# Kernel optimization log

Measured on AMD Instinct MI355X. Metric: run time of the kernel, lower is better.

The kernel has to match this reference:

```python
import jax, jax.numpy as jnp
import numpy as np

NEG_SLOPE = 0.2


def gat_layer(x, src, dst, W, a_src, a_dst, b, heads, out_c, concat):
    N = x.shape[0]
    h = (x @ W).reshape(N, heads, out_c)                      # [N,H,C]
    alpha_s = jnp.einsum('nhc,hc->nh', h, a_src)              # [N,H]
    alpha_d = jnp.einsum('nhc,hc->nh', h, a_dst)              # [N,H]
    e = jax.nn.leaky_relu(alpha_s[src] + alpha_d[dst], NEG_SLOPE)  # [E,H]
    # softmax over incoming edges per destination node (segment softmax)
    m = jax.ops.segment_max(e, dst, num_segments=N)
    m = jnp.where(jnp.isfinite(m), m, 0.0)
    ex = jnp.exp(e - m[dst])
    denom = jax.ops.segment_sum(ex, dst, num_segments=N)
    alpha = ex / (denom[dst] + 1e-16)                         # [E,H]
    out = jax.ops.segment_sum(alpha[:, :, None] * h[src], dst, num_segments=N)  # [N,H,C]
    out = out.reshape(N, heads * out_c) if concat else out.mean(axis=1)
    return out + b


def setup_inputs() -> dict:
    key = jax.random.key(0)
    ks = jax.random.split(key, 12)
    N, E, D, H, C, G = 20000, 160000, 256, 4, 128, 64
    x = jax.random.normal(ks[0], (N, D), dtype=jnp.float32)
    edge_index = jax.random.randint(ks[1], (2, E), 0, N)
    batch = jnp.sort(jax.random.randint(ks[2], (N,), 0, G))
    s = 0.05
    params = {
        'W1': jax.random.normal(ks[3], (D, H * C), jnp.float32) * s,
        'a_src1': jax.random.normal(ks[4], (H, C), jnp.float32) * s,
        'a_dst1': jax.random.normal(ks[5], (H, C), jnp.float32) * s,
        'b1': jnp.zeros((H * C,), jnp.float32),
        'W2': jax.random.normal(ks[6], (H * C, C), jnp.float32) * s,
        'a_src2': jax.random.normal(ks[7], (1, C), jnp.float32) * s,
        'a_dst2': jax.random.normal(ks[8], (1, C), jnp.float32) * s,
        'b2': jnp.zeros((C,), jnp.float32),
        'fc1_W': jax.random.normal(ks[9], (C, C // 2), jnp.float32) * s,
        'fc1_b': jnp.zeros((C // 2,), jnp.float32),
        'fc2_W': jax.random.normal(ks[10], (C // 2, 1), jnp.float32) * s,
        'fc2_b': jnp.zeros((1,), jnp.float32),
    }
    return dict(x=x, edge_index=edge_index, batch=batch, **params)


def reference(x, edge_index, batch, W1, a_src1, a_dst1, b1, W2, a_src2, a_dst2, b2,
              fc1_W, fc1_b, fc2_W, fc2_b):
    N = x.shape[0]
    G = 64  # number of graphs
    # add self-loops (PyG GATConv default)
    loop = jnp.arange(N, dtype=edge_index.dtype)
    src = jnp.concatenate([edge_index[0], loop])
    dst = jnp.concatenate([edge_index[1], loop])
    h = jax.nn.relu(gat_layer(x, src, dst, W1, a_src1, a_dst1, b1, 4, 128, True))
    h = gat_layer(h, src, dst, W2, a_src2, a_dst2, b2, 1, 128, False)
    # global mean pool per graph
    sums = jax.ops.segment_sum(h, batch, num_segments=G)
    cnts = jax.ops.segment_sum(jnp.ones((N,), h.dtype), batch, num_segments=G)
    pooled = sums / jnp.maximum(cnts, 1.0)[:, None]          # [G,128]
    out = jax.nn.relu(pooled @ fc1_W + fc1_b)
    return out @ fc2_W + fc2_b                                # [G,1]
```

## Files before the change

kernel.cpp:

```cpp
#include <hip/hip_runtime.h>
#include <hip/hip_bf16.h>
#include <cstdint>
#include <cstddef>

#define NEG_SLOPE 0.2f

typedef __attribute__((ext_vector_type(8))) __bf16 bf16x8;
typedef __attribute__((ext_vector_type(4))) __bf16 bf16x4;
typedef __attribute__((ext_vector_type(2))) __bf16 bf16x2;
typedef __attribute__((ext_vector_type(4))) float  f32x4;

__device__ __forceinline__ float lrelu(float v) {
    return (v < 0.f) ? NEG_SLOPE * v : v;
}

__device__ __forceinline__ unsigned fkey(float x) {
    unsigned b = __float_as_uint(x);
    return b ^ (unsigned)(((int)b >> 31) | 0x80000000);
}
__device__ __forceinline__ float funkey(unsigned k) {
    unsigned b = (k & 0x80000000u) ? (k ^ 0x80000000u) : ~k;
    return __uint_as_float(b);
}

__global__ __launch_bounds__(256) void gemm2_sum(
    const __bf16* __restrict__ A,
    const __bf16* __restrict__ Bt,
    __bf16* __restrict__ Cout,
    const float* __restrict__ ps_part, const float* __restrict__ pd_part,
    float* __restrict__ as2, float* __restrict__ ad2,
    unsigned* __restrict__ gmax2u,
    int M, int MB)
{
    if ((int)blockIdx.y >= MB) {
        int chunk = ((int)blockIdx.y - MB) * 2 + (int)blockIdx.x;
        int i = chunk * 256 + threadIdx.x;
        float lm = -1e30f;
        if (i < M) {
            float4 p = *(const float4*)&ps_part[(size_t)i * 4];
            float4 q = *(const float4*)&pd_part[(size_t)i * 4];
            float s = (p.x + p.y) + (p.z + p.w);
            float d = (q.x + q.y) + (q.z + q.w);
            as2[i] = s;
            ad2[i] = d;
            lm = s;
        }
        #pragma unroll
        for (int t = 1; t < 64; t <<= 1) lm = fmaxf(lm, __shfl_xor(lm, t));
        if ((threadIdx.x & 63) == 0) atomicMax(gmax2u, fkey(lm));
        return;
    }

    const int tid  = threadIdx.x;
    const int wave = tid >> 6, lane = tid & 63;
    const int wr = wave >> 1, wc = wave & 1;
    const int rowbase = blockIdx.y * 64 + wr * 32;
    const int colbase = blockIdx.x * 64 + wc * 32;
    const int l15 = lane & 15, kg = lane >> 4;
    const int K = 512, N = 128;

    size_t aoff[2], boff[2];
    #pragma unroll
    for (int mf = 0; mf < 2; ++mf) {
        int r = rowbase + mf * 16 + l15;
        if (r > M - 1) r = M - 1;
        aoff[mf] = (size_t)r * K + kg * 8;
    }
    #pragma unroll
    for (int nf = 0; nf < 2; ++nf) {
        int c = colbase + nf * 16 + l15;
        boff[nf] = (size_t)c * K + kg * 8;
    }

    f32x4 acc[2][2];
    #pragma unroll
    for (int mf = 0; mf < 2; ++mf)
        #pragma unroll
        for (int nf = 0; nf < 2; ++nf)
            acc[mf][nf] = (f32x4){0.f, 0.f, 0.f, 0.f};

    #pragma unroll 2
    for (int k0 = 0; k0 < K; k0 += 32) {
        bf16x8 af[2], bfr[2];
        #pragma unroll
        for (int mf = 0; mf < 2; ++mf)
            af[mf] = *(const bf16x8*)(A + aoff[mf] + k0);
        #pragma unroll
        for (int nf = 0; nf < 2; ++nf)
            bfr[nf] = *(const bf16x8*)(Bt + boff[nf] + k0);
        #pragma unroll
        for (int mf = 0; mf < 2; ++mf)
            #pragma unroll
            for (int nf = 0; nf < 2; ++nf)
                acc[mf][nf] = __builtin_amdgcn_mfma_f32_16x16x32_bf16(af[mf], bfr[nf], acc[mf][nf], 0, 0, 0);
    }

    #pragma unroll
    for (int mf = 0; mf < 2; ++mf)
        #pragma unroll
        for (int j = 0; j < 4; ++j) {
            int r = rowbase + mf * 16 + kg * 4 + j;
            if (r < M) {
                #pragma unroll
                for (int nf = 0; nf < 2; ++nf) {
                    int c = colbase + nf * 16 + l15;
                    Cout[(size_t)r * N + c] = (__bf16)acc[mf][nf][j];
                }
            }
        }
}

__global__ __launch_bounds__(256) void gemm1_agg(
    const __bf16* __restrict__ aggx,
    const __bf16* __restrict__ w1t,
    const float* __restrict__ b1, const float* __restrict__ wsd2,
    __bf16* __restrict__ out1b,
    float* __restrict__ ps_part, float* __restrict__ pd_part,
    int M)
{
    const int head = blockIdx.x;
    const int tid  = threadIdx.x;
    const int wave = tid >> 6, lane = tid & 63;
    const int wr = wave >> 1, wc = wave & 1;
    const int rowbase = blockIdx.y * 64 + wr * 32;
    const int l15 = lane & 15, kg = lane >> 4;

    size_t aoff[2], boff[4];
    #pragma unroll
    for (int mf = 0; mf < 2; ++mf) {
        int r = rowbase + mf * 16 + l15;
        if (r > M - 1) r = M - 1;
        aoff[mf] = (size_t)r * 1024 + head * 256 + kg * 8;
    }
    #pragma unroll
    for (int nf = 0; nf < 4; ++nf) {
        int c = head * 128 + wc * 64 + nf * 16 + l15;
        boff[nf] = (size_t)c * 256 + kg * 8;
    }

    f32x4 acc[2][4];
    #pragma unroll
    for (int mf = 0; mf < 2; ++mf)
        #pragma unroll
        for (int nf = 0; nf < 4; ++nf)
            acc[mf][nf] = (f32x4){0.f, 0.f, 0.f, 0.f};

    #pragma unroll 2
    for (int k0 = 0; k0 < 256; k0 += 32) {
        bf16x8 af[2], bfr[4];
        #pragma unroll
        for (int mf = 0; mf < 2; ++mf)
            af[mf] = *(const bf16x8*)(aggx + aoff[mf] + k0);
        #pragma unroll
        for (int nf = 0; nf < 4; ++nf)
            bfr[nf] = *(const bf16x8*)(w1t + boff[nf] + k0);
        #pragma unroll
        for (int mf = 0; mf < 2; ++mf)
            #pragma unroll
            for (int nf = 0; nf < 4; ++nf)
                acc[mf][nf] = __builtin_amdgcn_mfma_f32_16x16x32_bf16(af[mf], bfr[nf], acc[mf][nf], 0, 0, 0);
    }

    __shared__ float smp[2][64], smd[2][64];

    #pragma unroll
    for (int mf = 0; mf < 2; ++mf)
        #pragma unroll
        for (int j = 0; j < 4; ++j) {
            int r = rowbase + mf * 16 + kg * 4 + j;
            float ps = 0.f, pd = 0.f;
            #pragma unroll
            for (int nf = 0; nf < 4; ++nf) {
                int col = head * 128 + wc * 64 + nf * 16 + l15;
                float o = fmaxf(acc[mf][nf][j] + b1[col], 0.f);
                if (r < M)
                    out1b[(size_t)r * 512 + col] = (__bf16)o;
                ps = fmaf(o, wsd2[col], ps);
                pd = fmaf(o, wsd2[512 + col], pd);
            }
            #pragma unroll
            for (int t = 1; t < 16; t <<= 1) {
                ps += __shfl_xor(ps, t);
                pd += __shfl_xor(pd, t);
            }
            if (l15 == 0) {
                int lr = wr * 32 + mf * 16 + kg * 4 + j;
                smp[wc][lr] = ps;
                smd[wc][lr] = pd;
            }
        }
    __syncthreads();
    if (tid < 64) {
        int r = blockIdx.y * 64 + tid;
        if (r < M) {
            ps_part[(size_t)r * 4 + head] = smp[0][tid] + smp[1][tid];
            pd_part[(size_t)r * 4 + head] = smd[0][tid] + smd[1][tid];
        }
    }
}

__global__ void prep_kernel(const float* __restrict__ W1, const float* __restrict__ W2,
                            const float* __restrict__ as1w, const float* __restrict__ ad1w,
                            const float* __restrict__ as2w, const float* __restrict__ ad2w,
                            const int* __restrict__ batch,
                            __bf16* __restrict__ w1t, __bf16* __restrict__ w2t,
                            float* __restrict__ wsd1, float* __restrict__ wsd2,
                            int* __restrict__ gstart, int* __restrict__ cnt,
                            unsigned* __restrict__ gmax2u,
                            int N, int G)
{
    int t = blockIdx.x * 256 + threadIdx.x;
    if (t < 131072) {
        int i = t;
        int k = i >> 9, n = i & 511;
        w1t[n * 256 + k] = (__bf16)W1[i];
    } else if (t < 196608) {
        int j = t - 131072;
        int k = j >> 7, n = j & 127;
        w2t[n * 512 + k] = (__bf16)W2[j];
    } else if (t < 199680) {
        int t2 = t - 196608;
        if (t2 < 2048) {
            int k = t2 >> 3, v = t2 & 7, h = v >> 1;
            const float* av = (v & 1) ? (ad1w + h * 128) : (as1w + h * 128);
            float s = 0.f;
            for (int c = 0; c < 128; ++c) s += W1[k * 512 + h * 128 + c] * av[c];
            wsd1[v * 256 + k] = s;
        } else {
            int t3 = t2 - 2048;
            int k = t3 >> 1, v = t3 & 1;
            const float* av = v ? ad2w : as2w;
            float s = 0.f;
            for (int c = 0; c < 128; ++c) s += W2[k * 128 + c] * av[c];
            wsd2[v * 512 + k] = s;
        }
    } else if (t < 199680 + N) {
        int n = t - 199680;
        int b    = batch[n];
        int prev = (n == 0) ? -1 : batch[n - 1];
        for (int g = prev + 1; g <= b; ++g) gstart[g] = n;
        if (n == N - 1) {
            for (int g = b + 1; g <= G; ++g) gstart[g] = N;
        }
    } else if (t < 199680 + 2 * N) {
        cnt[t - 199680 - N] = 0;
    } else if (t == 199680 + 2 * N) {
        *gmax2u = fkey(-1e30f);
    }
}

__global__ __launch_bounds__(256) void count_cvtx(
    const int* __restrict__ ei, int* __restrict__ cnt,
    const float* __restrict__ x, const float* __restrict__ wsd1,
    __bf16* __restrict__ xb, float* __restrict__ as1_, float* __restrict__ ad1_,
    int ET, int E0, int N, int CB)
{
    if ((int)blockIdx.x < CB) {
        int base = (blockIdx.x * 256 + threadIdx.x) * 2;
        #pragma unroll
        for (int k = 0; k < 2; ++k) {
            int e = base + k;
            if (e < ET) {
                int d = (e < E0) ? ei[E0 + e] : (e - E0);
                atomicAdd(&cnt[d], 1);
            }
        }
        return;
    }
    int bid = blockIdx.x - CB;
    int wave = threadIdx.x >> 6, lane = threadIdx.x & 63;
    int n = bid * 4 + wave;
    if (n >= N) return;
    float4 xv = *(const float4*)&x[(size_t)n * 256 + lane * 4];
    bf16x4 xo;
    xo[0] = (__bf16)xv.x; xo[1] = (__bf16)xv.y; xo[2] = (__bf16)xv.z; xo[3] = (__bf16)xv.w;
    *(bf16x4*)&xb[(size_t)n * 256 + lane * 4] = xo;
    float p[8];
    #pragma unroll
    for (int v = 0; v < 8; ++v) {
        float4 wv = *(const float4*)&wsd1[v * 256 + lane * 4];
        p[v] = xv.x * wv.x + xv.y * wv.y + xv.z * wv.z + xv.w * wv.w;
    }
    #pragma unroll
    for (int v = 0; v < 8; ++v)
        #pragma unroll
        for (int s = 1; s < 64; s <<= 1) p[v] += __shfl_xor(p[v], s);
    if (lane == 0) {
        #pragma unroll
        for (int h = 0; h < 4; ++h) {
            as1_[n * 4 + h] = p[2 * h];
            ad1_[n * 4 + h] = p[2 * h + 1];
        }
    }
}

__global__ __launch_bounds__(1024) void scan_gmax(
    const int* __restrict__ cnt, int* __restrict__ offs, int* __restrict__ cur,
    const float* __restrict__ as1_, float* __restrict__ gmax1, int n)
{
    constexpr int CHUNK = 20;
    int t = threadIdx.x;
    int base = t * CHUNK;
    int v[CHUNK];
    int s = 0;
    #pragma unroll
    for (int i = 0; i < CHUNK; ++i) {
        int idx = base + i;
        int xv = (idx < n) ? cnt[idx] : 0;
        v[i] = s; s += xv;
    }
    int lane = t & 63, w = t >> 6;
    int sc = s;
    #pragma unroll
    for (int d = 1; d < 64; d <<= 1) {
        int o = __shfl_up(sc, d);
        if (lane >= d) sc += o;
    }
    __shared__ int wt[16], wb[17];
    __shared__ float gsm[16][4];
    if (lane == 63) wt[w] = sc;
    __syncthreads();
    if (t == 0) {
        int acc = 0;
        for (int i = 0; i < 16; ++i) { wb[i] = acc; acc += wt[i]; }
        wb[16] = acc;
    }
    __syncthreads();
    int ebase = wb[w] + (sc - s);
    #pragma unroll
    for (int i = 0; i < CHUNK; ++i) {
        int idx = base + i;
        if (idx < n) {
            int o = ebase + v[i];
            offs[idx] = o;
            cur[idx]  = o;
        }
    }
    if (t == 0) offs[n] = wb[16];

    float lm0 = -1e30f, lm1 = -1e30f, lm2 = -1e30f, lm3 = -1e30f;
    for (int i = t; i < n; i += 1024) {
        float4 a = *(const float4*)&as1_[(size_t)i * 4];
        lm0 = fmaxf(lm0, a.x); lm1 = fmaxf(lm1, a.y);
        lm2 = fmaxf(lm2, a.z); lm3 = fmaxf(lm3, a.w);
    }
    #pragma unroll
    for (int d = 1; d < 64; d <<= 1) {
        lm0 = fmaxf(lm0, __shfl_xor(lm0, d));
        lm1 = fmaxf(lm1, __shfl_xor(lm1, d));
        lm2 = fmaxf(lm2, __shfl_xor(lm2, d));
        lm3 = fmaxf(lm3, __shfl_xor(lm3, d));
    }
    if (lane == 0) {
        gsm[w][0] = lm0; gsm[w][1] = lm1; gsm[w][2] = lm2; gsm[w][3] = lm3;
    }
    __syncthreads();
    if (t == 0) {
        float m0 = -1e30f, m1 = -1e30f, m2 = -1e30f, m3 = -1e30f;
        for (int i = 0; i < 16; ++i) {
            m0 = fmaxf(m0, gsm[i][0]); m1 = fmaxf(m1, gsm[i][1]);
            m2 = fmaxf(m2, gsm[i][2]); m3 = fmaxf(m3, gsm[i][3]);
        }
        gmax1[0] = m0; gmax1[1] = m1; gmax1[2] = m2; gmax1[3] = m3;
    }
}

__global__ void scatter_kernel(const int* __restrict__ ei, int* __restrict__ cur,
                               int* __restrict__ srcs, int ET, int E0)
{
    int e = blockIdx.x * blockDim.x + threadIdx.x;
    if (e >= ET) return;
    int d = (e < E0) ? ei[E0 + e] : (e - E0);
    int s = (e < E0) ? ei[e] : (e - E0);
    int pos = atomicAdd(&cur[d], 1);
    srcs[pos] = s;
}

__global__ __launch_bounds__(256) void aggx_kernel(
    const __bf16* __restrict__ xb, const int* __restrict__ offs,
    const int* __restrict__ srcs,
    const float* __restrict__ as1_, const float* __restrict__ ad1_,
    const float* __restrict__ gmax1,
    __bf16* __restrict__ aggx, int N)
{
    __shared__ float w4s[4][64][4];
    __shared__ int   sidx[4][64];
    int wave = threadIdx.x >> 6, lane = threadIdx.x & 63;
    int n = blockIdx.x * 4 + wave;
    if (n >= N) return;
    int s0 = offs[n], s1 = offs[n + 1];
    float4 adv = *(const float4*)&ad1_[(size_t)n * 4];
    float m0 = lrelu(gmax1[0] + adv.x);
    float m1 = lrelu(gmax1[1] + adv.y);
    float m2 = lrelu(gmax1[2] + adv.z);
    float m3 = lrelu(gmax1[3] + adv.w);

    float d0 = 0.f, d1 = 0.f, d2 = 0.f, d3 = 0.f;
    float a0[4] = {0.f,0.f,0.f,0.f}, a1[4] = {0.f,0.f,0.f,0.f};
    float a2[4] = {0.f,0.f,0.f,0.f}, a3[4] = {0.f,0.f,0.f,0.f};
    const __bf16* xbase = xb + lane * 4;

    for (int base = s0; base < s1; base += 64) {
        int cnt = min(64, s1 - base);
        if (lane < cnt) {
            int s = srcs[base + lane];
            float4 av = *(const float4*)&as1_[(size_t)s * 4];
            float w0 = __expf(lrelu(av.x + adv.x) - m0);
            float w1 = __expf(lrelu(av.y + adv.y) - m1);
            float w2 = __expf(lrelu(av.z + adv.z) - m2);
            float w3 = __expf(lrelu(av.w + adv.w) - m3);
            d0 += w0; d1 += w1; d2 += w2; d3 += w3;
            sidx[wave][lane] = s;
            w4s[wave][lane][0] = w0; w4s[wave][lane][1] = w1;
            w4s[wave][lane][2] = w2; w4s[wave][lane][3] = w3;
        }
        int j = 0;
        for (; j + 7 < cnt; j += 8) {
            int s_[8]; float4 w_[8]; bf16x4 xv_[8];
            #pragma unroll
            for (int i = 0; i < 8; ++i) {
                s_[i] = sidx[wave][j + i];
                w_[i] = *(const float4*)&w4s[wave][j + i][0];
            }
            #pragma unroll
            for (int i = 0; i < 8; ++i)
                xv_[i] = *(const bf16x4*)(xbase + (size_t)s_[i] * 256);
            #pragma unroll
            for (int i = 0; i < 8; ++i) {
                float xf[4];
                #pragma unroll
                for (int c = 0; c < 4; ++c) xf[c] = (float)xv_[i][c];
                #pragma unroll
                for (int c = 0; c < 4; ++c) {
                    a0[c] = fmaf(w_[i].x, xf[c], a0[c]);
                    a1[c] = fmaf(w_[i].y, xf[c], a1[c]);
                    a2[c] = fmaf(w_[i].z, xf[c], a2[c]);
                    a3[c] = fmaf(w_[i].w, xf[c], a3[c]);
                }
            }
        }
        for (; j < cnt; ++j) {
            int s = sidx[wave][j];
            float4 w = *(const float4*)&w4s[wave][j][0];
            bf16x4 xv = *(const bf16x4*)(xbase + (size_t)s * 256);
            float xf[4];
            #pragma unroll
            for (int c = 0; c < 4; ++c) xf[c] = (float)xv[c];
            #pragma unroll
            for (int c = 0; c < 4; ++c) {
                a0[c] = fmaf(w.x, xf[c], a0[c]);
                a1[c] = fmaf(w.y, xf[c], a1[c]);
                a2[c] = fmaf(w.z, xf[c], a2[c]);
                a3[c] = fmaf(w.w, xf[c], a3[c]);
            }
        }
    }

    #pragma unroll
    for (int t = 1; t < 64; t <<= 1) {
        d0 += __shfl_xor(d0, t);
        d1 += __shfl_xor(d1, t);
        d2 += __shfl_xor(d2, t);
        d3 += __shfl_xor(d3, t);
    }

    float i0 = 1.f / (d0 + 1e-16f);
    float i1 = 1.f / (d1 + 1e-16f);
    float i2 = 1.f / (d2 + 1e-16f);
    float i3 = 1.f / (d3 + 1e-16f);
    __bf16* obase = aggx + (size_t)n * 1024 + lane * 4;
    bf16x4 o;
    #pragma unroll
    for (int c = 0; c < 4; ++c) o[c] = (__bf16)(a0[c] * i0);
    *(bf16x4*)(obase + 0)   = o;
    #pragma unroll
    for (int c = 0; c < 4; ++c) o[c] = (__bf16)(a1[c] * i1);
    *(bf16x4*)(obase + 256) = o;
    #pragma unroll
    for (int c = 0; c < 4; ++c) o[c] = (__bf16)(a2[c] * i2);
    *(bf16x4*)(obase + 512) = o;
    #pragma unroll
    for (int c = 0; c < 4; ++c) o[c] = (__bf16)(a3[c] * i3);
    *(bf16x4*)(obase + 768) = o;
}

__global__ __launch_bounds__(256) void aggregate2_kernel(
    const __bf16* __restrict__ h2b, const int* __restrict__ offs,
    const int* __restrict__ srcs,
    const float* __restrict__ as2, const float* __restrict__ ad2,
    const unsigned* __restrict__ gmax2u,
    const float* __restrict__ b2, float* __restrict__ out2, int N)
{
    __shared__ float wls[4][64];
    __shared__ int   sidx[4][64];
    int wave = threadIdx.x >> 6, lane = threadIdx.x & 63;
    int n = blockIdx.x * 4 + wave;
    if (n >= N) return;
    int s0 = offs[n], s1 = offs[n + 1];
    float adn = ad2[n];
    float m = lrelu(funkey(*gmax2u) + adn);

    float den = 0.f;
    float c0 = 0.f, c1 = 0.f;
    const __bf16* hbase = h2b + lane * 2;

    for (int base = s0; base < s1; base += 64) {
        int cnt = min(64, s1 - base);
        if (lane < cnt) {
            int s = srcs[base + lane];
            float w = __expf(lrelu(as2[s] + adn) - m);
            den += w;
            sidx[wave][lane] = s;
            wls[wave][lane]  = w;
        }
        int j = 0;
        for (; j + 7 < cnt; j += 8) {
            int s_[8]; float w_[8]; bf16x2 h_[8];
            #pragma unroll
            for (int i = 0; i < 8; ++i) {
                s_[i] = sidx[wave][j + i];
                w_[i] = wls[wave][j + i];
            }
            #pragma unroll
            for (int i = 0; i < 8; ++i)
                h_[i] = *(const bf16x2*)(hbase + (size_t)s_[i] * 128);
            #pragma unroll
            for (int i = 0; i < 8; ++i) {
                c0 = fmaf(w_[i], (float)h_[i][0], c0);
                c1 = fmaf(w_[i], (float)h_[i][1], c1);
            }
        }
        for (; j < cnt; ++j) {
            int s = sidx[wave][j];
            float w = wls[wave][j];
            bf16x2 hv = *(const bf16x2*)(hbase + (size_t)s * 128);
            c0 = fmaf(w, (float)hv[0], c0);
            c1 = fmaf(w, (float)hv[1], c1);
        }
    }

    #pragma unroll
    for (int t = 1; t < 64; t <<= 1) den += __shfl_xor(den, t);
    float inv = 1.f / (den + 1e-16f);
    float2 o;
    o.x = c0 * inv + b2[lane * 2 + 0];
    o.y = c1 * inv + b2[lane * 2 + 1];
    *(float2*)&out2[(size_t)n * 128 + lane * 2] = o;
}

#define POOL_S 16
__global__ void pool_stage1(const float* __restrict__ out2, const int* __restrict__ gstart,
                            float* __restrict__ partial, int C)
{
    int g = blockIdx.x, slice = blockIdx.y;
    int c = threadIdx.x;
    int s = gstart[g], e = gstart[g + 1];
    int len = e - s;
    int chunk = (len + POOL_S - 1) / POOL_S;
    int n0 = s + slice * chunk;
    int n1 = min(n0 + chunk, e);
    float acc = 0.f;
    for (int n = n0; n < n1; ++n) acc += out2[(size_t)n * C + c];
    partial[((size_t)g * POOL_S + slice) * C + c] = acc;
}

__global__ __launch_bounds__(128) void pool_head(
    const float* __restrict__ partial, const int* __restrict__ gstart,
    const float* __restrict__ fc1W, const float* __restrict__ fc1b,
    const float* __restrict__ fc2W, const float* __restrict__ fc2b,
    float* __restrict__ out)
{
    int g = blockIdx.x;
    int t = threadIdx.x;
    __shared__ float pl[128];
    float acc = 0.f;
    #pragma unroll
    for (int s = 0; s < POOL_S; ++s)
        acc += partial[((size_t)g * POOL_S + s) * 128 + t];
    float cntf = (float)(gstart[g + 1] - gstart[g]);
    pl[t] = acc / fmaxf(cntf, 1.0f);
    __syncthreads();
    if (t < 64) {
        float v = 0.f;
        for (int c = 0; c < 128; ++c)
            v += pl[c] * fc1W[c * 64 + t];
        v = fmaxf(v + fc1b[t], 0.f) * fc2W[t];
        #pragma unroll
        for (int s = 32; s > 0; s >>= 1) v += __shfl_down(v, s);
        if (t == 0) out[g] = v + fc2b[0];
    }
}

extern "C" void kernel_launch(void* const* d_in, const int* in_sizes, int n_in,
                              void* d_out, int out_size, void* d_ws, size_t ws_size,
                              hipStream_t stream)
{
    const float* x    = (const float*)d_in[0];
    const int*   ei   = (const int*)d_in[1];
    const int*   batch= (const int*)d_in[2];
    const float* W1   = (const float*)d_in[3];
    const float* as1w = (const float*)d_in[4];
    const float* ad1w = (const float*)d_in[5];
    const float* b1   = (const float*)d_in[6];
    const float* W2   = (const float*)d_in[7];
    const float* as2w = (const float*)d_in[8];
    const float* ad2w = (const float*)d_in[9];
    const float* b2   = (const float*)d_in[10];
    const float* fc1W = (const float*)d_in[11];
    const float* fc1b = (const float*)d_in[12];
    const float* fc2W = (const float*)d_in[13];
    const float* fc2b = (const float*)d_in[14];
    float* out = (float*)d_out;

    const int D = 256, C = 128, G = 64;
    const int N  = in_sizes[0] / D;
    const int E0 = in_sizes[1] / 2;
    const int ET = E0 + N;

    char* p = (char*)d_ws;
    auto alloc = [&](size_t bytes) -> char* {
        char* r = p;
        p += (bytes + 255) & ~(size_t)255;
        return r;
    };
    __bf16* xb    = (__bf16*)alloc((size_t)N * D * 2);
    __bf16* aggx  = (__bf16*)alloc((size_t)N * 4 * 256 * 2);
    __bf16* out1b = (__bf16*)alloc((size_t)N * 512 * 2);
    __bf16* h2b   = (__bf16*)alloc((size_t)N * C * 2);
    float*  out2  = (float*)alloc((size_t)N * C * 4);
    __bf16* w1t   = (__bf16*)alloc((size_t)256 * 512 * 2);
    __bf16* w2t   = (__bf16*)alloc((size_t)512 * 128 * 2);
    float* wsd1   = (float*)alloc(8 * 256 * 4);
    float* wsd2   = (float*)alloc(2 * 512 * 4);
    float* gmax1  = (float*)alloc(4 * 4);
    unsigned* gmax2u = (unsigned*)alloc(4);
    float* as1_   = (float*)alloc((size_t)N * 4 * 4);
    float* ad1_   = (float*)alloc((size_t)N * 4 * 4);
    float* ps_part= (float*)alloc((size_t)N * 4 * 4);
    float* pd_part= (float*)alloc((size_t)N * 4 * 4);
    float* as2    = (float*)alloc((size_t)N * 4);
    float* ad2    = (float*)alloc((size_t)N * 4);
    int*   cnt    = (int*)alloc((size_t)N * 4);
    int*   cur    = (int*)alloc((size_t)N * 4);
    int*   offs   = (int*)alloc((size_t)(N + 1) * 4);
    int*   srcs   = (int*)alloc((size_t)ET * 4);
    int*   gstart = (int*)alloc((size_t)(G + 1) * 4);
    float* partial= (float*)alloc((size_t)G * POOL_S * C * 4);

    {
        int total = 199680 + 2 * N + 1;
        prep_kernel<<<(total + 255) / 256, 256, 0, stream>>>(
            W1, W2, as1w, ad1w, as2w, ad2w, batch,
            w1t, w2t, wsd1, wsd2, gstart, cnt, gmax2u, N, G);
    }

    {
        int CB = (ET + 511) / 512;
        count_cvtx<<<CB + N / 4, 256, 0, stream>>>(
            ei, cnt, x, wsd1, xb, as1_, ad1_, ET, E0, N, CB);
    }

    scan_gmax<<<1, 1024, 0, stream>>>(cnt, offs, cur, as1_, gmax1, N);

    scatter_kernel<<<(ET + 255) / 256, 256, 0, stream>>>(ei, cur, srcs, ET, E0);

    aggx_kernel<<<(N + 3) / 4, 256, 0, stream>>>(
        xb, offs, srcs, as1_, ad1_, gmax1, aggx, N);

    gemm1_agg<<<dim3(4, (N + 63) / 64), 256, 0, stream>>>(
        aggx, w1t, b1, wsd2, out1b, ps_part, pd_part, N);

    {
        int MB = (N + 63) / 64;
        int SB = ((N + 255) / 256 + 1) / 2;
        gemm2_sum<<<dim3(2, MB + SB), 256, 0, stream>>>(
            out1b, w2t, h2b, ps_part, pd_part, as2, ad2, gmax2u, N, MB);
    }

    aggregate2_kernel<<<(N + 3) / 4, 256, 0, stream>>>(
        h2b, offs, srcs, as2, ad2, gmax2u, b2, out2, N);

    pool_stage1<<<dim3(G, POOL_S), C, 0, stream>>>(out2, gstart, partial, C);
    pool_head<<<G, 128, 0, stream>>>(partial, gstart, fc1W, fc1b, fc2W, fc2b, out);
}
```

Before: 194.0 us.

## Fuse layer-1 neighbor aggregation with per-head GEMM through shared memory

Merges the aggregation kernel and the first GEMM into one kernel. Each block aggregates 16 destination nodes for all four heads into an LDS tile, then each wave runs the MFMA GEMM for one head. This removes the N×1024 bf16 aggx round trip through global memory and one kernel launch. In exchange the GEMM tile is only 16 rows, so each block reloads W1 slices with less reuse, and the sequential per-wave aggregation of four nodes may leave waves unbalanced before the barrier.

```diff
diff --git a/kernel.cpp b/kernel.cpp
--- a/kernel.cpp
+++ b/kernel.cpp
@@ -21,6 +21,173 @@
 __device__ __forceinline__ float funkey(unsigned k) {
     unsigned b = (k & 0x80000000u) ? (k ^ 0x80000000u) : ~k;
     return __uint_as_float(b);
+}
+
+__global__ __launch_bounds__(256) void agg_gemm1(
+    const __bf16* __restrict__ xb, const int* __restrict__ offs,
+    const int* __restrict__ srcs,
+    const float* __restrict__ as1_, const float* __restrict__ ad1_,
+    const float* __restrict__ gmax1,
+    const __bf16* __restrict__ w1t,
+    const float* __restrict__ b1, const float* __restrict__ wsd2,
+    __bf16* __restrict__ out1b,
+    float* __restrict__ ps_part, float* __restrict__ pd_part,
+    int N)
+{
+    __shared__ __bf16 axs[4][16][260];
+    __shared__ float w4s[4][64][4];
+    __shared__ int   sidx[4][64];
+
+    const int tid  = threadIdx.x;
+    const int wave = tid >> 6, lane = tid & 63;
+    const int tile = blockIdx.x * 16;
+
+    for (int i = 0; i < 4; ++i) {
+        int nn = wave * 4 + i;
+        int n  = tile + nn;
+        if (n >= N) break;
+        int s0 = offs[n], s1 = offs[n + 1];
+        float4 adv = *(const float4*)&ad1_[(size_t)n * 4];
+        float m0 = lrelu(gmax1[0] + adv.x);
+        float m1 = lrelu(gmax1[1] + adv.y);
+        float m2 = lrelu(gmax1[2] + adv.z);
+        float m3 = lrelu(gmax1[3] + adv.w);
+
+        float d0 = 0.f, d1 = 0.f, d2 = 0.f, d3 = 0.f;
+        float a0[4] = {0.f,0.f,0.f,0.f}, a1[4] = {0.f,0.f,0.f,0.f};
+        float a2[4] = {0.f,0.f,0.f,0.f}, a3[4] = {0.f,0.f,0.f,0.f};
+        const __bf16* xbase = xb + lane * 4;
+
+        for (int base = s0; base < s1; base += 64) {
+            int cnt = min(64, s1 - base);
+            if (lane < cnt) {
+                int s = srcs[base + lane];
+                float4 av = *(const float4*)&as1_[(size_t)s * 4];
+                float w0 = __expf(lrelu(av.x + adv.x) - m0);
+                float w1 = __expf(lrelu(av.y + adv.y) - m1);
+                float w2 = __expf(lrelu(av.z + adv.z) - m2);
+                float w3 = __expf(lrelu(av.w + adv.w) - m3);
+                d0 += w0; d1 += w1; d2 += w2; d3 += w3;
+                sidx[wave][lane] = s;
+                w4s[wave][lane][0] = w0; w4s[wave][lane][1] = w1;
+                w4s[wave][lane][2] = w2; w4s[wave][lane][3] = w3;
+            }
+            int j = 0;
+            for (; j + 7 < cnt; j += 8) {
+                int s_[8]; float4 w_[8]; bf16x4 xv_[8];
+                #pragma unroll
+                for (int q = 0; q < 8; ++q) {
+                    s_[q] = sidx[wave][j + q];
+                    w_[q] = *(const float4*)&w4s[wave][j + q][0];
+                }
+                #pragma unroll
+                for (int q = 0; q < 8; ++q)
+                    xv_[q] = *(const bf16x4*)(xbase + (size_t)s_[q] * 256);
+                #pragma unroll
+                for (int q = 0; q < 8; ++q) {
+                    float xf[4];
+                    #pragma unroll
+                    for (int c = 0; c < 4; ++c) xf[c] = (float)xv_[q][c];
+                    #pragma unroll
+                    for (int c = 0; c < 4; ++c) {
+                        a0[c] = fmaf(w_[q].x, xf[c], a0[c]);
+                        a1[c] = fmaf(w_[q].y, xf[c], a1[c]);
+                        a2[c] = fmaf(w_[q].z, xf[c], a2[c]);
+                        a3[c] = fmaf(w_[q].w, xf[c], a3[c]);
+                    }
+                }
+            }
+            for (; j < cnt; ++j) {
+                int s = sidx[wave][j];
+                float4 w = *(const float4*)&w4s[wave][j][0];
+                bf16x4 xv = *(const bf16x4*)(xbase + (size_t)s * 256);
+                float xf[4];
+                #pragma unroll
+                for (int c = 0; c < 4; ++c) xf[c] = (float)xv[c];
+                #pragma unroll
+                for (int c = 0; c < 4; ++c) {
+                    a0[c] = fmaf(w.x, xf[c], a0[c]);
+                    a1[c] = fmaf(w.y, xf[c], a1[c]);
+                    a2[c] = fmaf(w.z, xf[c], a2[c]);
+                    a3[c] = fmaf(w.w, xf[c], a3[c]);
+                }
+            }
+        }
+
+        #pragma unroll
+        for (int t = 1; t < 64; t <<= 1) {
+            d0 += __shfl_xor(d0, t);
+            d1 += __shfl_xor(d1, t);
+            d2 += __shfl_xor(d2, t);
+            d3 += __shfl_xor(d3, t);
+        }
+        float i0 = 1.f / (d0 + 1e-16f);
+        float i1 = 1.f / (d1 + 1e-16f);
+        float i2 = 1.f / (d2 + 1e-16f);
+        float i3 = 1.f / (d3 + 1e-16f);
+        bf16x4 o;
+        #pragma unroll
+        for (int c = 0; c < 4; ++c) o[c] = (__bf16)(a0[c] * i0);
+        *(bf16x4*)&axs[0][nn][lane * 4] = o;
+        #pragma unroll
+        for (int c = 0; c < 4; ++c) o[c] = (__bf16)(a1[c] * i1);
+        *(bf16x4*)&axs[1][nn][lane * 4] = o;
+        #pragma unroll
+        for (int c = 0; c < 4; ++c) o[c] = (__bf16)(a2[c] * i2);
+        *(bf16x4*)&axs[2][nn][lane * 4] = o;
+        #pragma unroll
+        for (int c = 0; c < 4; ++c) o[c] = (__bf16)(a3[c] * i3);
+        *(bf16x4*)&axs[3][nn][lane * 4] = o;
+    }
+    __syncthreads();
+
+    const int head = wave;
+    const int l15 = lane & 15, kg = lane >> 4;
+
+    f32x4 acc[8];
+    #pragma unroll
+    for (int nf = 0; nf < 8; ++nf) acc[nf] = (f32x4){0.f, 0.f, 0.f, 0.f};
+
+    #pragma unroll 2
+    for (int k0 = 0; k0 < 256; k0 += 32) {
+        bf16x4 alo = *(const bf16x4*)&axs[head][l15][k0 + kg * 8];
+        bf16x4 ahi = *(const bf16x4*)&axs[head][l15][k0 + kg * 8 + 4];
+        bf16x8 af;
+        #pragma unroll
+        for (int c = 0; c < 4; ++c) { af[c] = alo[c]; af[4 + c] = ahi[c]; }
+        bf16x8 bfr[8];
+        #pragma unroll
+        for (int nf = 0; nf < 8; ++nf)
+            bfr[nf] = *(const bf16x8*)(w1t + (size_t)(head * 128 + nf * 16 + l15) * 256 + k0 + kg * 8);
+        #pragma unroll
+        for (int nf = 0; nf < 8; ++nf)
+            acc[nf] = __builtin_amdgcn_mfma_f32_16x16x32_bf16(af, bfr[nf], acc[nf], 0, 0, 0);
+    }
+
+    #pragma unroll
+    for (int j = 0; j < 4; ++j) {
+        int nn = kg * 4 + j;
+        int r  = tile + nn;
+        float ps = 0.f, pd = 0.f;
+        #pragma unroll
+        for (int nf = 0; nf < 8; ++nf) {
+            int col = head * 128 + nf * 16 + l15;
+            float o = fmaxf(acc[nf][j] + b1[col], 0.f);
+            if (r < N)
+                out1b[(size_t)r * 512 + col] = (__bf16)o;
+            ps = fmaf(o, wsd2[col], ps);
+            pd = fmaf(o, wsd2[512 + col], pd);
+        }
+        #pragma unroll
+        for (int t = 1; t < 16; t <<= 1) {
+            ps += __shfl_xor(ps, t);
+            pd += __shfl_xor(pd, t);
+        }
+        if (l15 == 0 && r < N) {
+            ps_part[(size_t)r * 4 + head] = ps;
+            pd_part[(size_t)r * 4 + head] = pd;
+        }
+    }
 }
 
 __global__ __launch_bounds__(256) void gemm2_sum(
@@ -108,95 +275,6 @@
                 }
             }
         }
-}
-
-__global__ __launch_bounds__(256) void gemm1_agg(
-    const __bf16* __restrict__ aggx,
-    const __bf16* __restrict__ w1t,
-    const float* __restrict__ b1, const float* __restrict__ wsd2,
-    __bf16* __restrict__ out1b,
-    float* __restrict__ ps_part, float* __restrict__ pd_part,
-    int M)
-{
-    const int head = blockIdx.x;
-    const int tid  = threadIdx.x;
-    const int wave = tid >> 6, lane = tid & 63;
-    const int wr = wave >> 1, wc = wave & 1;
-    const int rowbase = blockIdx.y * 64 + wr * 32;
-    const int l15 = lane & 15, kg = lane >> 4;
-
-    size_t aoff[2], boff[4];
-    #pragma unroll
-    for (int mf = 0; mf < 2; ++mf) {
-        int r = rowbase + mf * 16 + l15;
-        if (r > M - 1) r = M - 1;
-        aoff[mf] = (size_t)r * 1024 + head * 256 + kg * 8;
-    }
-    #pragma unroll
-    for (int nf = 0; nf < 4; ++nf) {
-        int c = head * 128 + wc * 64 + nf * 16 + l15;
-        boff[nf] = (size_t)c * 256 + kg * 8;
-    }
-
-    f32x4 acc[2][4];
-    #pragma unroll
-    for (int mf = 0; mf < 2; ++mf)
-        #pragma unroll
-        for (int nf = 0; nf < 4; ++nf)
-            acc[mf][nf] = (f32x4){0.f, 0.f, 0.f, 0.f};
-
-    #pragma unroll 2
-    for (int k0 = 0; k0 < 256; k0 += 32) {
-        bf16x8 af[2], bfr[4];
-        #pragma unroll
-        for (int mf = 0; mf < 2; ++mf)
-            af[mf] = *(const bf16x8*)(aggx + aoff[mf] + k0);
-        #pragma unroll
-        for (int nf = 0; nf < 4; ++nf)
-            bfr[nf] = *(const bf16x8*)(w1t + boff[nf] + k0);
-        #pragma unroll
-        for (int mf = 0; mf < 2; ++mf)
-            #pragma unroll
-            for (int nf = 0; nf < 4; ++nf)
-                acc[mf][nf] = __builtin_amdgcn_mfma_f32_16x16x32_bf16(af[mf], bfr[nf], acc[mf][nf], 0, 0, 0);
-    }
-
-    __shared__ float smp[2][64], smd[2][64];
-
-    #pragma unroll
-    for (int mf = 0; mf < 2; ++mf)
-        #pragma unroll
-        for (int j = 0; j < 4; ++j) {
-            int r = rowbase + mf * 16 + kg * 4 + j;
-            float ps = 0.f, pd = 0.f;
-            #pragma unroll
-            for (int nf = 0; nf < 4; ++nf) {
-                int col = head * 128 + wc * 64 + nf * 16 + l15;
-                float o = fmaxf(acc[mf][nf][j] + b1[col], 0.f);
-                if (r < M)
-                    out1b[(size_t)r * 512 + col] = (__bf16)o;
-                ps = fmaf(o, wsd2[col], ps);
-                pd = fmaf(o, wsd2[512 + col], pd);
-            }
-            #pragma unroll
-            for (int t = 1; t < 16; t <<= 1) {
-                ps += __shfl_xor(ps, t);
-                pd += __shfl_xor(pd, t);
-            }
-            if (l15 == 0) {
-                int lr = wr * 32 + mf * 16 + kg * 4 + j;
-                smp[wc][lr] = ps;
-                smd[wc][lr] = pd;
-            }
-        }
-    __syncthreads();
-    if (tid < 64) {
-        int r = blockIdx.y * 64 + tid;
-        if (r < M) {
-            ps_part[(size_t)r * 4 + head] = smp[0][tid] + smp[1][tid];
-            pd_part[(size_t)r * 4 + head] = smd[0][tid] + smd[1][tid];
-        }
-    }
 }
 
 __global__ void prep_kernel(const float* __restrict__ W1, const float* __restrict__ W2,
@@ -376,114 +454,6 @@
     srcs[pos] = s;
 }
 
-__global__ __launch_bounds__(256) void aggx_kernel(
-    const __bf16* __restrict__ xb, const int* __restrict__ offs,
-    const int* __restrict__ srcs,
-    const float* __restrict__ as1_, const float* __restrict__ ad1_,
-    const float* __restrict__ gmax1,
-    __bf16* __restrict__ aggx, int N)
-{
-    __shared__ float w4s[4][64][4];
-    __shared__ int   sidx[4][64];
-    int wave = threadIdx.x >> 6, lane = threadIdx.x & 63;
-    int n = blockIdx.x * 4 + wave;
-    if (n >= N) return;
-    int s0 = offs[n], s1 = offs[n + 1];
-    float4 adv = *(const float4*)&ad1_[(size_t)n * 4];
-    float m0 = lrelu(gmax1[0] + adv.x);
-    float m1 = lrelu(gmax1[1] + adv.y);
-    float m2 = lrelu(gmax1[2] + adv.z);
-    float m3 = lrelu(gmax1[3] + adv.w);
-
-    float d0 = 0.f, d1 = 0.f, d2 = 0.f, d3 = 0.f;
-    float a0[4] = {0.f,0.f,0.f,0.f}, a1[4] = {0.f,0.f,0.f,0.f};
-    float a2[4] = {0.f,0.f,0.f,0.f}, a3[4] = {0.f,0.f,0.f,0.f};
-    const __bf16* xbase = xb + lane * 4;
-
-    for (int base = s0; base < s1; base += 64) {
-        int cnt = min(64, s1 - base);
-        if (lane < cnt) {
-            int s = srcs[base + lane];
-            float4 av = *(const float4*)&as1_[(size_t)s * 4];
-            float w0 = __expf(lrelu(av.x + adv.x) - m0);
-            float w1 = __expf(lrelu(av.y + adv.y) - m1);
-            float w2 = __expf(lrelu(av.z + adv.z) - m2);
-            float w3 = __expf(lrelu(av.w + adv.w) - m3);
-            d0 += w0; d1 += w1; d2 += w2; d3 += w3;
-            sidx[wave][lane] = s;
-            w4s[wave][lane][0] = w0; w4s[wave][lane][1] = w1;
-            w4s[wave][lane][2] = w2; w4s[wave][lane][3] = w3;
-        }
-        int j = 0;
-        for (; j + 7 < cnt; j += 8) {
-            int s_[8]; float4 w_[8]; bf16x4 xv_[8];
-            #pragma unroll
-            for (int i = 0; i < 8; ++i) {
-                s_[i] = sidx[wave][j + i];
-                w_[i] = *(const float4*)&w4s[wave][j + i][0];
-            }
-            #pragma unroll
-            for (int i = 0; i < 8; ++i)
-                xv_[i] = *(const bf16x4*)(xbase + (size_t)s_[i] * 256);
-            #pragma unroll
-            for (int i = 0; i < 8; ++i) {
-                float xf[4];
-                #pragma unroll
-                for (int c = 0; c < 4; ++c) xf[c] = (float)xv_[i][c];
-                #pragma unroll
-                for (int c = 0; c < 4; ++c) {
-                    a0[c] = fmaf(w_[i].x, xf[c], a0[c]);
-                    a1[c] = fmaf(w_[i].y, xf[c], a1[c]);
-                    a2[c] = fmaf(w_[i].z, xf[c], a2[c]);
-                    a3[c] = fmaf(w_[i].w, xf[c], a3[c]);
-                }
-            }
-        }
-        for (; j < cnt; ++j) {
-            int s = sidx[wave][j];
-            float4 w = *(const float4*)&w4s[wave][j][0];
-            bf16x4 xv = *(const bf16x4*)(xbase + (size_t)s * 256);
-            float xf[4];
-            #pragma unroll
-            for (int c = 0; c < 4; ++c) xf[c] = (float)xv[c];
-            #pragma unroll
-            for (int c = 0; c < 4; ++c) {
-                a0[c] = fmaf(w.x, xf[c], a0[c]);
-                a1[c] = fmaf(w.y, xf[c], a1[c]);
-                a2[c] = fmaf(w.z, xf[c], a2[c]);
-                a3[c] = fmaf(w.w, xf[c], a3[c]);
-            }
-        }
-    }
-
-    #pragma unroll
-    for (int t = 1; t < 64; t <<= 1) {
-        d0 += __shfl_xor(d0, t);
-        d1 += __shfl_xor(d1, t);
-        d2 += __shfl_xor(d2, t);
-        d3 += __shfl_xor(d3, t);
-    }
-
-    float i0 = 1.f / (d0 + 1e-16f);
-    float i1 = 1.f / (d1 + 1e-16f);
-    float i2 = 1.f / (d2 + 1e-16f);
-    float i3 = 1.f / (d3 + 1e-16f);
-    __bf16* obase = aggx + (size_t)n * 1024 + lane * 4;
-    bf16x4 o;
-    #pragma unroll
-    for (int c = 0; c < 4; ++c) o[c] = (__bf16)(a0[c] * i0);
-    *(bf16x4*)(obase + 0)   = o;
-    #pragma unroll
-    for (int c = 0; c < 4; ++c) o[c] = (__bf16)(a1[c] * i1);
-    *(bf16x4*)(obase + 256) = o;
-    #pragma unroll
-    for (int c = 0; c < 4; ++c) o[c] = (__bf16)(a2[c] * i2);
-    *(bf16x4*)(obase + 512) = o;
-    #pragma unroll
-    for (int c = 0; c < 4; ++c) o[c] = (__bf16)(a3[c] * i3);
-    *(bf16x4*)(obase + 768) = o;
-}
-
 __global__ __launch_bounds__(256) void aggregate2_kernel(
     const __bf16* __restrict__ h2b, const int* __restrict__ offs,
     const int* __restrict__ srcs,
@@ -624,7 +594,6 @@
         return r;
     };
     __bf16* xb    = (__bf16*)alloc((size_t)N * D * 2);
-    __bf16* aggx  = (__bf16*)alloc((size_t)N * 4 * 256 * 2);
     __bf16* out1b = (__bf16*)alloc((size_t)N * 512 * 2);
     __bf16* h2b   = (__bf16*)alloc((size_t)N * C * 2);
     float*  out2  = (float*)alloc((size_t)N * C * 4);
@@ -664,11 +633,9 @@
 
     scatter_kernel<<<(ET + 255) / 256, 256, 0, stream>>>(ei, cur, srcs, ET, E0);
 
-    aggx_kernel<<<(N + 3) / 4, 256, 0, stream>>>(
-        xb, offs, srcs, as1_, ad1_, gmax1, aggx, N);
-
-    gemm1_agg<<<dim3(4, (N + 63) / 64), 256, 0, stream>>>(
-        aggx, w1t, b1, wsd2, out1b, ps_part, pd_part, N);
+    agg_gemm1<<<(N + 15) / 16, 256, 0, stream>>>(
+        xb, offs, srcs, as1_, ad1_, gmax1, w1t, b1, wsd2,
+        out1b, ps_part, pd_part, N);
 
     {
         int MB = (N + 63) / 64;
```

Result: slower. 207.1 us (+6.7%).
